# Performance work log

Measured on AMD Instinct MI355X. Metric: run time of the kernel, lower is better.

## Reference

```python
import jax, jax.numpy as jnp
import numpy as np

G = 8          # num_groups
GIN = 2048 // G   # group_in_features
GOUT = 2048 // G  # group_out_features


def setup_inputs() -> dict:
    key = jax.random.key(0)
    kx, kw, kb = jax.random.split(key, 3)
    x = jax.random.normal(kx, (8192, 2048), dtype=jnp.float32)
    # per-group linear params, torch nn.Linear default init scale ~ U(-1/sqrt(fan_in), ...)
    bound = 1.0 / np.sqrt(GIN)
    W = jax.random.uniform(kw, (G, GIN, GOUT), minval=-bound, maxval=bound, dtype=jnp.float32)
    b = jax.random.uniform(kb, (G, GOUT), minval=-bound, maxval=bound, dtype=jnp.float32)
    # rational activation coeffs, init p=[1,0,0,0], q=[1,0,0] per group
    p = jnp.tile(jnp.array([1.0, 0.0, 0.0, 0.0], dtype=jnp.float32), (G, 1))
    q = jnp.tile(jnp.array([1.0, 0.0, 0.0], dtype=jnp.float32), (G, 1))
    return {"x": x, "W": W, "b": b, "p": p, "q": q}


def _rational(y, p, q):
    # y: [N, G, GOUT]; p: [G, 4]; q: [G, 3] -> broadcast over N and GOUT
    p = p[None, :, :, None]  # [1,G,4,1]
    q = q[None, :, :, None]  # [1,G,3,1]
    y2 = y * y
    y3 = y2 * y
    num = p[:, :, 0] + p[:, :, 1] * y + p[:, :, 2] * y2 + p[:, :, 3] * y3
    den = 1.0 + jnp.abs(q[:, :, 0] * y + q[:, :, 1] * y2 + q[:, :, 2] * y3)
    return num / den


def reference(x, W, b, p, q):
    N = x.shape[0]
    xg = x.reshape(N, G, GIN)                       # chunk along last dim
    y = jnp.einsum('ngi,gio->ngo', xg, W) + b[None]  # grouped GEMM, [N,G,GOUT]
    out = _rational(y, p, q)
    return out.reshape(N, G * GOUT)                 # cat along last dim
```

## Files before the change

kernel.cpp:

```cpp
#include <hip/hip_runtime.h>
#include <hip/hip_bf16.h>

#define G_ 8
#define GIN_ 256
#define GOUT_ 256
#define NROWS_ 8192
#define LDX_ 2048

typedef __attribute__((ext_vector_type(4))) float f32x4;
typedef __attribute__((ext_vector_type(8))) short bf16x8;

__global__ __launch_bounds__(256) void wprep_kernel(const float* __restrict__ W,
                                                    __hip_bfloat16* __restrict__ Wt) {
    __shared__ float tile[64][65];
    const int bid = blockIdx.x;
    const int g  = bid >> 4;
    const int kt = (bid >> 2) & 3;
    const int ct = bid & 3;
    const float* Wg = W + g * (GIN_ * GOUT_);
    __hip_bfloat16* Wo = Wt + (size_t)g * (GIN_ * GOUT_);
    const int lane_o = threadIdx.x & 63;
    const int sub    = threadIdx.x >> 6;
#pragma unroll
    for (int r = 0; r < 16; ++r) {
        int i = r * 4 + sub;
        tile[i][lane_o] = Wg[(kt * 64 + i) * GOUT_ + ct * 64 + lane_o];
    }
    __syncthreads();
    const int col = threadIdx.x & 63;
    const int kgb = threadIdx.x >> 6;
#pragma unroll
    for (int h = 0; h < 2; ++h) {
        const int kg    = kgb + h * 4;
        const int kglob = kt * 64 + kg * 8;
        const int c     = kglob >> 5;
        const int quad  = (kglob >> 3) & 3;
        const int colg  = ct * 64 + col;
        const int cb    = colg >> 4;
        const int c16   = colg & 15;
        union { __hip_bfloat16 hh[8]; bf16x8 v; } cv;
#pragma unroll
        for (int j = 0; j < 8; ++j)
            cv.hh[j] = __float2bfloat16(tile[kg * 8 + j][col]);
        *(bf16x8*)(Wo + (size_t)(c * 16 + cb) * 512 + c16 * 32 + quad * 8) = cv.v;
    }
}

__device__ __forceinline__ bf16x8 cvt8(const f32x4 a, const f32x4 b) {
    union { __hip_bfloat16 h[8]; bf16x8 v; } u;
    u.h[0] = __float2bfloat16(a.x); u.h[1] = __float2bfloat16(a.y);
    u.h[2] = __float2bfloat16(a.z); u.h[3] = __float2bfloat16(a.w);
    u.h[4] = __float2bfloat16(b.x); u.h[5] = __float2bfloat16(b.y);
    u.h[6] = __float2bfloat16(b.z); u.h[7] = __float2bfloat16(b.w);
    return u.v;
}

__global__ __launch_bounds__(512, 8) void gkan_kernel(const float* __restrict__ x,
                                                      const __hip_bfloat16* __restrict__ Wt,
                                                      const float* __restrict__ bias,
                                                      const float* __restrict__ pc,
                                                      const float* __restrict__ qc,
                                                      float* __restrict__ out) {
    __shared__ __align__(16) float As[32 * 256];

    const int bid  = blockIdx.x;
    const int g    = bid & 7;
    const int row0 = (bid >> 3) * 32;

    const int t    = threadIdx.x;
    const int wave = t >> 6;
    const int lane = t & 63;
    const int lm   = lane & 15;
    const int q    = lane >> 4;

    {
        const float* xrow = x + (size_t)row0 * LDX_ + g * GIN_;
#pragma unroll
        for (int r = 0; r < 4; ++r) {
            const int row  = r * 8 + wave;
            const int gidx = lane ^ wave;
            const float* src = xrow + (size_t)row * LDX_ + gidx * 4;
            __builtin_amdgcn_global_load_lds(
                (const __attribute__((address_space(1))) void*)src,
                (__attribute__((address_space(3))) void*)((char*)As + r * 8192 + t * 16),
                16, 0, 0);
        }
    }

    asm volatile("s_waitcnt vmcnt(0) lgkmcnt(0)\n\ts_barrier" ::: "memory");

    f32x4 acc[2][2] = {};
    const __hip_bfloat16* bp = Wt + (size_t)g * (GIN_ * GOUT_)
                                  + (wave * 2) * 512 + lm * 32 + q * 8;
#pragma unroll 1
    for (int c = 0; c < 8; ++c) {
        const bf16x8 bf0 = *(const bf16x8*)(bp);
        const bf16x8 bf1 = *(const bf16x8*)(bp + 512);
        const int s0 = c * 8 + q * 2;
        bf16x8 af[2];
#pragma unroll
        for (int mt = 0; mt < 2; ++mt) {
            const int rr = mt * 16 + lm;
            const f32x4 lo = *(const f32x4*)(As + rr * 256 + ((s0 ^ (lm & 7)) * 4));
            const f32x4 hi = *(const f32x4*)(As + rr * 256 + (((s0 + 1) ^ (lm & 7)) * 4));
            af[mt] = cvt8(lo, hi);
        }
        acc[0][0] = __builtin_amdgcn_mfma_f32_16x16x32_bf16(bf0, af[0], acc[0][0], 0, 0, 0);
        acc[0][1] = __builtin_amdgcn_mfma_f32_16x16x32_bf16(bf1, af[0], acc[0][1], 0, 0, 0);
        acc[1][0] = __builtin_amdgcn_mfma_f32_16x16x32_bf16(bf0, af[1], acc[1][0], 0, 0, 0);
        acc[1][1] = __builtin_amdgcn_mfma_f32_16x16x32_bf16(bf1, af[1], acc[1][1], 0, 0, 0);
        bp += 16 * 512;
    }

    const float p0 = pc[g * 4 + 0], p1 = pc[g * 4 + 1];
    const float p2 = pc[g * 4 + 2], p3 = pc[g * 4 + 3];
    const float q0 = qc[g * 3 + 0], q1 = qc[g * 3 + 1], q2 = qc[g * 3 + 2];

#pragma unroll
    for (int mt = 0; mt < 2; ++mt) {
        const int row_o = row0 + mt * 16 + lm;
#pragma unroll
        for (int nt = 0; nt < 2; ++nt) {
            const int col0 = g * GOUT_ + wave * 32 + nt * 16 + q * 4;
            const f32x4 bb4 = *(const f32x4*)(bias + col0);
            f32x4 o;
#pragma unroll
            for (int r = 0; r < 4; ++r) {
                const float y   = acc[mt][nt][r] + bb4[r];
                const float num = p0 + y * (p1 + y * (p2 + y * p3));
                const float den = 1.0f + fabsf(y * (q0 + y * (q1 + y * q2)));
                o[r] = num * __builtin_amdgcn_rcpf(den);
            }
            *(f32x4*)(out + (size_t)row_o * LDX_ + col0) = o;
        }
    }
}

extern "C" void kernel_launch(void* const* d_in, const int* in_sizes, int n_in,
                              void* d_out, int out_size, void* d_ws, size_t ws_size,
                              hipStream_t stream) {
    const float* x = (const float*)d_in[0];
    const float* W = (const float*)d_in[1];
    const float* b = (const float*)d_in[2];
    const float* p = (const float*)d_in[3];
    const float* q = (const float*)d_in[4];
    float* out = (float*)d_out;

    __hip_bfloat16* Wt = (__hip_bfloat16*)d_ws;

    wprep_kernel<<<128, 256, 0, stream>>>(W, Wt);
    gkan_kernel<<<2048, 512, 0, stream>>>(x, Wt, b, p, q, out);
}
```

Measured before the change: 134.4 us.

## Split K into two halves and prefetch B fragments to overlap loads with MFMA

Hoists the bf16 weight-fragment loads ahead of the x tile copy into registers, and reorganises the global-to-LDS copy so each half of K lands in its own LDS region. Compute on the first half starts after a partial vmcnt wait while the second half is still in flight, and the second-half B fragments are loaded during the first half's MFMAs. The occupancy hint drops from 8 to 6 waves-per-EU to make room for the extra fragment registers. The cost is more register pressure, lower occupancy, and waitcnt counts that depend on the exact order of issued loads.

```diff
diff --git a/kernel.cpp b/kernel.cpp
--- a/kernel.cpp
+++ b/kernel.cpp
@@ -55,7 +55,7 @@
     return u.v;
 }
 
-__global__ __launch_bounds__(512, 8) void gkan_kernel(const float* __restrict__ x,
+__global__ __launch_bounds__(512, 6) void gkan_kernel(const float* __restrict__ x,
                                                       const __hip_bfloat16* __restrict__ Wt,
                                                       const float* __restrict__ bias,
                                                       const float* __restrict__ pc,
@@ -73,43 +73,80 @@
     const int lm   = lane & 15;
     const int q    = lane >> 4;
 
+    const __hip_bfloat16* bp = Wt + (size_t)g * (GIN_ * GOUT_)
+                                  + (wave * 2) * 512 + lm * 32 + q * 8;
+    bf16x8 B0[4], B1[4];
+#pragma unroll
+    for (int c = 0; c < 4; ++c) {
+        B0[c] = *(const bf16x8*)(bp + (size_t)c * (16 * 512));
+        B1[c] = *(const bf16x8*)(bp + (size_t)c * (16 * 512) + 512);
+    }
+
     {
         const float* xrow = x + (size_t)row0 * LDX_ + g * GIN_;
+        const int rw  = t >> 5;
+        const int g8  = t & 7;
+        const int ghi = t & 24;
 #pragma unroll
-        for (int r = 0; r < 4; ++r) {
-            const int row  = r * 8 + wave;
-            const int gidx = lane ^ wave;
-            const float* src = xrow + (size_t)row * LDX_ + gidx * 4;
-            __builtin_amdgcn_global_load_lds(
-                (const __attribute__((address_space(1))) void*)src,
-                (__attribute__((address_space(3))) void*)((char*)As + r * 8192 + t * 16),
-                16, 0, 0);
-        }
+        for (int h = 0; h < 2; ++h)
+#pragma unroll
+            for (int j = 0; j < 2; ++j) {
+                const int row  = j * 16 + rw;
+                const int gsrc = h * 32 + ghi + (g8 ^ (row & 7));
+                const float* src = xrow + (size_t)row * LDX_ + gsrc * 4;
+                __builtin_amdgcn_global_load_lds(
+                    (const __attribute__((address_space(1))) void*)src,
+                    (__attribute__((address_space(3))) void*)
+                        ((char*)As + h * 16384 + j * 8192 + t * 16),
+                    16, 0, 0);
+            }
     }
 
-    asm volatile("s_waitcnt vmcnt(0) lgkmcnt(0)\n\ts_barrier" ::: "memory");
+    asm volatile("s_waitcnt vmcnt(2)\n\ts_barrier" ::: "memory");
 
     f32x4 acc[2][2] = {};
-    const __hip_bfloat16* bp = Wt + (size_t)g * (GIN_ * GOUT_)
-                                  + (wave * 2) * 512 + lm * 32 + q * 8;
-#pragma unroll 1
-    for (int c = 0; c < 8; ++c) {
-        const bf16x8 bf0 = *(const bf16x8*)(bp);
-        const bf16x8 bf1 = *(const bf16x8*)(bp + 512);
-        const int s0 = c * 8 + q * 2;
+#pragma unroll
+    for (int c = 0; c < 4; ++c) {
         bf16x8 af[2];
 #pragma unroll
         for (int mt = 0; mt < 2; ++mt) {
-            const int rr = mt * 16 + lm;
-            const f32x4 lo = *(const f32x4*)(As + rr * 256 + ((s0 ^ (lm & 7)) * 4));
-            const f32x4 hi = *(const f32x4*)(As + rr * 256 + (((s0 + 1) ^ (lm & 7)) * 4));
+            const int rr  = mt * 16 + lm;
+            const int gg0 = c * 8 + ((q * 2)     ^ (lm & 7));
+            const int gg1 = c * 8 + ((q * 2 + 1) ^ (lm & 7));
+            const f32x4 lo = *(const f32x4*)((const char*)As + rr * 512 + gg0 * 16);
+            const f32x4 hi = *(const f32x4*)((const char*)As + rr * 512 + gg1 * 16);
             af[mt] = cvt8(lo, hi);
         }
-        acc[0][0] = __builtin_amdgcn_mfma_f32_16x16x32_bf16(bf0, af[0], acc[0][0], 0, 0, 0);
-        acc[0][1] = __builtin_amdgcn_mfma_f32_16x16x32_bf16(bf1, af[0], acc[0][1], 0, 0, 0);
-        acc[1][0] = __builtin_amdgcn_mfma_f32_16x16x32_bf16(bf0, af[1], acc[1][0], 0, 0, 0);
-        acc[1][1] = __builtin_amdgcn_mfma_f32_16x16x32_bf16(bf1, af[1], acc[1][1], 0, 0, 0);
-        bp += 16 * 512;
+        acc[0][0] = __builtin_amdgcn_mfma_f32_16x16x32_bf16(B0[c], af[0], acc[0][0], 0, 0, 0);
+        acc[0][1] = __builtin_amdgcn_mfma_f32_16x16x32_bf16(B1[c], af[0], acc[0][1], 0, 0, 0);
+        acc[1][0] = __builtin_amdgcn_mfma_f32_16x16x32_bf16(B0[c], af[1], acc[1][0], 0, 0, 0);
+        acc[1][1] = __builtin_amdgcn_mfma_f32_16x16x32_bf16(B1[c], af[1], acc[1][1], 0, 0, 0);
+    }
+
+#pragma unroll
+    for (int c = 0; c < 4; ++c) {
+        B0[c] = *(const bf16x8*)(bp + (size_t)(c + 4) * (16 * 512));
+        B1[c] = *(const bf16x8*)(bp + (size_t)(c + 4) * (16 * 512) + 512);
+    }
+
+    asm volatile("s_waitcnt vmcnt(8)\n\ts_barrier" ::: "memory");
+
+#pragma unroll
+    for (int c = 0; c < 4; ++c) {
+        bf16x8 af[2];
+#pragma unroll
+        for (int mt = 0; mt < 2; ++mt) {
+            const int rr  = mt * 16 + lm;
+            const int gg0 = c * 8 + ((q * 2)     ^ (lm & 7));
+            const int gg1 = c * 8 + ((q * 2 + 1) ^ (lm & 7));
+            const f32x4 lo = *(const f32x4*)((const char*)As + 16384 + rr * 512 + gg0 * 16);
+            const f32x4 hi = *(const f32x4*)((const char*)As + 16384 + rr * 512 + gg1 * 16);
+            af[mt] = cvt8(lo, hi);
+        }
+        acc[0][0] = __builtin_amdgcn_mfma_f32_16x16x32_bf16(B0[c], af[0], acc[0][0], 0, 0, 0);
+        acc[0][1] = __builtin_amdgcn_mfma_f32_16x16x32_bf16(B1[c], af[0], acc[0][1], 0, 0, 0);
+        acc[1][0] = __builtin_amdgcn_mfma_f32_16x16x32_bf16(B0[c], af[1], acc[1][0], 0, 0, 0);
+        acc[1][1] = __builtin_amdgcn_mfma_f32_16x16x32_bf16(B1[c], af[1], acc[1][1], 0, 0, 0);
     }
 
     const float p0 = pc[g * 4 + 0], p1 = pc[g * 4 + 1];
```

Measured after the change: 134.1 us. No clear change (-0.2%).

## Restructure GEMM so each block covers all groups for 16 full rows

Applied to the files above, without the earlier changes.

Each block now loads 16 full rows of x (all 8 groups) through registers, converts them to bf16 once, and stores them to a swizzled LDS tile. Each wave then handles one group and computes all 256 output columns in two passes of 8 MFMA accumulators. Before, x was kept as fp32 in LDS and converted on every read. The grid shrinks from 2048 to 512 blocks and the occupancy hint drops, so there is less latency hiding and more register pressure. It also drops the async global-to-LDS load path and reads far more W per wave from global or L2.

```diff
diff --git a/kernel.cpp b/kernel.cpp
--- a/kernel.cpp
+++ b/kernel.cpp
@@ -9,6 +9,10 @@
 
 typedef __attribute__((ext_vector_type(4))) float f32x4;
 typedef __attribute__((ext_vector_type(8))) short bf16x8;
+
+__device__ __forceinline__ void lds_barrier() {
+    asm volatile("s_waitcnt lgkmcnt(0)\n\ts_barrier" ::: "memory");
+}
 
 __global__ __launch_bounds__(256) void wprep_kernel(const float* __restrict__ W,
                                                     __hip_bfloat16* __restrict__ Wt) {
@@ -46,92 +50,84 @@
     }
 }
 
-__device__ __forceinline__ bf16x8 cvt8(const f32x4 a, const f32x4 b) {
-    union { __hip_bfloat16 h[8]; bf16x8 v; } u;
-    u.h[0] = __float2bfloat16(a.x); u.h[1] = __float2bfloat16(a.y);
-    u.h[2] = __float2bfloat16(a.z); u.h[3] = __float2bfloat16(a.w);
-    u.h[4] = __float2bfloat16(b.x); u.h[5] = __float2bfloat16(b.y);
-    u.h[6] = __float2bfloat16(b.z); u.h[7] = __float2bfloat16(b.w);
-    return u.v;
-}
-
-__global__ __launch_bounds__(512, 8) void gkan_kernel(const float* __restrict__ x,
+__global__ __launch_bounds__(512, 4) void gkan_kernel(const float* __restrict__ x,
                                                       const __hip_bfloat16* __restrict__ Wt,
                                                       const float* __restrict__ bias,
                                                       const float* __restrict__ pc,
                                                       const float* __restrict__ qc,
                                                       float* __restrict__ out) {
-    __shared__ __align__(16) float As[32 * 256];
+    __shared__ __align__(16) __hip_bfloat16 As[16 * 2048];
 
     const int bid  = blockIdx.x;
-    const int g    = bid & 7;
-    const int row0 = (bid >> 3) * 32;
+    const int row0 = bid * 16;
 
     const int t    = threadIdx.x;
-    const int wave = t >> 6;
+    const int w    = t >> 6;
     const int lane = t & 63;
     const int lm   = lane & 15;
     const int q    = lane >> 4;
 
     {
-        const float* xrow = x + (size_t)row0 * LDX_ + g * GIN_;
+        const float* xb = x + (size_t)row0 * LDX_ + t * 4;
+        f32x4 v[16];
 #pragma unroll
-        for (int r = 0; r < 4; ++r) {
-            const int row  = r * 8 + wave;
-            const int gidx = lane ^ wave;
-            const float* src = xrow + (size_t)row * LDX_ + gidx * 4;
-            __builtin_amdgcn_global_load_lds(
-                (const __attribute__((address_space(1))) void*)src,
-                (__attribute__((address_space(3))) void*)((char*)As + r * 8192 + t * 16),
-                16, 0, 0);
+        for (int r = 0; r < 16; ++r)
+            v[r] = *(const f32x4*)(xb + (size_t)r * LDX_);
+
+        const int gk   = t >> 1;
+        const int half = t & 1;
+#pragma unroll
+        for (int i = 0; i < 16; ++i) {
+            const int r = i ^ (gk & 7);
+            union { __hip_bfloat16 h[4]; uint2 u2; } cv;
+            cv.h[0] = __float2bfloat16(v[r].x);
+            cv.h[1] = __float2bfloat16(v[r].y);
+            cv.h[2] = __float2bfloat16(v[r].z);
+            cv.h[3] = __float2bfloat16(v[r].w);
+            const int phys = (gk & ~7) | ((gk & 7) ^ (r & 7));
+            *(uint2*)((char*)As + r * 4096 + phys * 16 + half * 8) = cv.u2;
         }
     }
+    lds_barrier();
 
-    asm volatile("s_waitcnt vmcnt(0) lgkmcnt(0)\n\ts_barrier" ::: "memory");
+    const float p0 = pc[w * 4 + 0], p1 = pc[w * 4 + 1];
+    const float p2 = pc[w * 4 + 2], p3 = pc[w * 4 + 3];
+    const float q0 = qc[w * 3 + 0], q1 = qc[w * 3 + 1], q2 = qc[w * 3 + 2];
 
-    f32x4 acc[2][2] = {};
-    const __hip_bfloat16* bp = Wt + (size_t)g * (GIN_ * GOUT_)
-                                  + (wave * 2) * 512 + lm * 32 + q * 8;
+    const char* ab = (const char*)As + lm * 4096 + w * 512;
+
 #pragma unroll 1
-    for (int c = 0; c < 8; ++c) {
-        const bf16x8 bf0 = *(const bf16x8*)(bp);
-        const bf16x8 bf1 = *(const bf16x8*)(bp + 512);
-        const int s0 = c * 8 + q * 2;
-        bf16x8 af[2];
+    for (int p = 0; p < 2; ++p) {
+        f32x4 acc[8] = {};
+        const __hip_bfloat16* bp = Wt + (size_t)w * (GIN_ * GOUT_)
+                                      + (size_t)(p * 8) * 512 + lm * 32 + q * 8;
+#pragma unroll 1
+        for (int c = 0; c < 8; ++c) {
+            const int gg   = c * 4 + q;
+            const int phys = (gg & 24) | ((gg & 7) ^ (lm & 7));
+            const bf16x8 af = *(const bf16x8*)(ab + phys * 16);
+            const __hip_bfloat16* bc = bp + (size_t)c * (16 * 512);
 #pragma unroll
-        for (int mt = 0; mt < 2; ++mt) {
-            const int rr = mt * 16 + lm;
-            const f32x4 lo = *(const f32x4*)(As + rr * 256 + ((s0 ^ (lm & 7)) * 4));
-            const f32x4 hi = *(const f32x4*)(As + rr * 256 + (((s0 + 1) ^ (lm & 7)) * 4));
-            af[mt] = cvt8(lo, hi);
+            for (int nt = 0; nt < 8; ++nt) {
+                const bf16x8 bf = *(const bf16x8*)(bc + nt * 512);
+                acc[nt] = __builtin_amdgcn_mfma_f32_16x16x32_bf16(bf, af, acc[nt], 0, 0, 0);
+            }
         }
-        acc[0][0] = __builtin_amdgcn_mfma_f32_16x16x32_bf16(bf0, af[0], acc[0][0], 0, 0, 0);
-        acc[0][1] = __builtin_amdgcn_mfma_f32_16x16x32_bf16(bf1, af[0], acc[0][1], 0, 0, 0);
-        acc[1][0] = __builtin_amdgcn_mfma_f32_16x16x32_bf16(bf0, af[1], acc[1][0], 0, 0, 0);
-        acc[1][1] = __builtin_amdgcn_mfma_f32_16x16x32_bf16(bf1, af[1], acc[1][1], 0, 0, 0);
-        bp += 16 * 512;
-    }
 
-    const float p0 = pc[g * 4 + 0], p1 = pc[g * 4 + 1];
-    const float p2 = pc[g * 4 + 2], p3 = pc[g * 4 + 3];
-    const float q0 = qc[g * 3 + 0], q1 = qc[g * 3 + 1], q2 = qc[g * 3 + 2];
-
+        const int colb = w * GOUT_ + p * 128;
 #pragma unroll
-    for (int mt = 0; mt < 2; ++mt) {
-        const int row_o = row0 + mt * 16 + lm;
-#pragma unroll
-        for (int nt = 0; nt < 2; ++nt) {
-            const int col0 = g * GOUT_ + wave * 32 + nt * 16 + q * 4;
+        for (int nt = 0; nt < 8; ++nt) {
+            const int col0 = colb + nt * 16 + q * 4;
             const f32x4 bb4 = *(const f32x4*)(bias + col0);
             f32x4 o;
 #pragma unroll
             for (int r = 0; r < 4; ++r) {
-                const float y   = acc[mt][nt][r] + bb4[r];
+                const float y   = acc[nt][r] + bb4[r];
                 const float num = p0 + y * (p1 + y * (p2 + y * p3));
                 const float den = 1.0f + fabsf(y * (q0 + y * (q1 + y * q2)));
                 o[r] = num * __builtin_amdgcn_rcpf(den);
             }
-            *(f32x4*)(out + (size_t)row_o * LDX_ + col0) = o;
+            *(f32x4*)(out + (size_t)(row0 + lm) * LDX_ + col0) = o;
         }
     }
 }
@@ -149,5 +145,5 @@
     __hip_bfloat16* Wt = (__hip_bfloat16*)d_ws;
 
     wprep_kernel<<<128, 256, 0, stream>>>(W, Wt);
-    gkan_kernel<<<2048, 512, 0, stream>>>(x, Wt, b, p, q, out);
+    gkan_kernel<<<512, 512, 0, stream>>>(x, Wt, b, p, q, out);
 }
```

Result: slower. 187.9 us (+39.8%).

## Double-buffer x slabs per block and keep W fragments in registers

Applied to the files above, without the earlier changes.

Each block now handles 128 rows as four 32-row slabs instead of a single slab. The next slab is prefetched into a second LDS buffer with global_load_lds while the current one is computed and its epilogue stored. The block's W fragments, bias and rational coefficients are loaded into registers once and reused across all four slabs, which cuts redundant weight loads. In exchange the grid shrinks to a quarter, so there are fewer blocks per CU and less latency hiding from occupancy, and register and LDS use per block rise.

```diff
diff --git a/kernel.cpp b/kernel.cpp
--- a/kernel.cpp
+++ b/kernel.cpp
@@ -55,17 +55,17 @@
     return u.v;
 }
 
-__global__ __launch_bounds__(512, 8) void gkan_kernel(const float* __restrict__ x,
+__global__ __launch_bounds__(512, 4) void gkan_kernel(const float* __restrict__ x,
                                                       const __hip_bfloat16* __restrict__ Wt,
                                                       const float* __restrict__ bias,
                                                       const float* __restrict__ pc,
                                                       const float* __restrict__ qc,
                                                       float* __restrict__ out) {
-    __shared__ __align__(16) float As[32 * 256];
+    __shared__ __align__(16) float As[2][32 * 256];
 
     const int bid  = blockIdx.x;
     const int g    = bid & 7;
-    const int row0 = (bid >> 3) * 32;
+    const int row0 = (bid >> 3) * 128;
 
     const int t    = threadIdx.x;
     const int wave = t >> 6;
@@ -73,67 +73,94 @@
     const int lm   = lane & 15;
     const int q    = lane >> 4;
 
-    {
-        const float* xrow = x + (size_t)row0 * LDX_ + g * GIN_;
-#pragma unroll
-        for (int r = 0; r < 4; ++r) {
-            const int row  = r * 8 + wave;
-            const int gidx = lane ^ wave;
-            const float* src = xrow + (size_t)row * LDX_ + gidx * 4;
-            __builtin_amdgcn_global_load_lds(
-                (const __attribute__((address_space(1))) void*)src,
-                (__attribute__((address_space(3))) void*)((char*)As + r * 8192 + t * 16),
-                16, 0, 0);
-        }
+    const float* xbase = x + (size_t)row0 * LDX_ + g * GIN_;
+    const int gsrc = (lane & ~7) | ((lane & 7) ^ wave);
+
+#define DMA_SLAB(s, buf)                                                      \
+    {                                                                         \
+        const float* xs_ = xbase + (size_t)(s) * 32 * LDX_;                   \
+        _Pragma("unroll")                                                     \
+        for (int r_ = 0; r_ < 4; ++r_) {                                      \
+            const float* src_ = xs_ + (size_t)(r_ * 8 + wave) * LDX_ + gsrc * 4; \
+            __builtin_amdgcn_global_load_lds(                                 \
+                (const __attribute__((address_space(1))) void*)src_,          \
+                (__attribute__((address_space(3))) void*)                     \
+                    ((char*)As + (buf) * 32768 + r_ * 8192 + t * 16),         \
+                16, 0, 0);                                                    \
+        }                                                                     \
     }
 
-    asm volatile("s_waitcnt vmcnt(0) lgkmcnt(0)\n\ts_barrier" ::: "memory");
+    DMA_SLAB(0, 0);
 
-    f32x4 acc[2][2] = {};
     const __hip_bfloat16* bp = Wt + (size_t)g * (GIN_ * GOUT_)
                                   + (wave * 2) * 512 + lm * 32 + q * 8;
-#pragma unroll 1
+    bf16x8 B0[8], B1[8];
+#pragma unroll
     for (int c = 0; c < 8; ++c) {
-        const bf16x8 bf0 = *(const bf16x8*)(bp);
-        const bf16x8 bf1 = *(const bf16x8*)(bp + 512);
-        const int s0 = c * 8 + q * 2;
-        bf16x8 af[2];
-#pragma unroll
-        for (int mt = 0; mt < 2; ++mt) {
-            const int rr = mt * 16 + lm;
-            const f32x4 lo = *(const f32x4*)(As + rr * 256 + ((s0 ^ (lm & 7)) * 4));
-            const f32x4 hi = *(const f32x4*)(As + rr * 256 + (((s0 + 1) ^ (lm & 7)) * 4));
-            af[mt] = cvt8(lo, hi);
-        }
-        acc[0][0] = __builtin_amdgcn_mfma_f32_16x16x32_bf16(bf0, af[0], acc[0][0], 0, 0, 0);
-        acc[0][1] = __builtin_amdgcn_mfma_f32_16x16x32_bf16(bf1, af[0], acc[0][1], 0, 0, 0);
-        acc[1][0] = __builtin_amdgcn_mfma_f32_16x16x32_bf16(bf0, af[1], acc[1][0], 0, 0, 0);
-        acc[1][1] = __builtin_amdgcn_mfma_f32_16x16x32_bf16(bf1, af[1], acc[1][1], 0, 0, 0);
-        bp += 16 * 512;
+        B0[c] = *(const bf16x8*)(bp + (size_t)c * (16 * 512));
+        B1[c] = *(const bf16x8*)(bp + (size_t)c * (16 * 512) + 512);
     }
 
+    f32x4 bb4[2];
+    int col0[2];
+#pragma unroll
+    for (int nt = 0; nt < 2; ++nt) {
+        col0[nt] = g * GOUT_ + wave * 32 + nt * 16 + q * 4;
+        bb4[nt]  = *(const f32x4*)(bias + col0[nt]);
+    }
     const float p0 = pc[g * 4 + 0], p1 = pc[g * 4 + 1];
     const float p2 = pc[g * 4 + 2], p3 = pc[g * 4 + 3];
     const float q0 = qc[g * 3 + 0], q1 = qc[g * 3 + 1], q2 = qc[g * 3 + 2];
 
+    asm volatile("s_waitcnt vmcnt(0)\n\ts_barrier" ::: "memory");
+
+#pragma unroll 1
+    for (int s = 0; s < 4; ++s) {
+        const int buf = s & 1;
+
+        if (s < 3) DMA_SLAB(s + 1, buf ^ 1);
+
+        f32x4 acc[2][2] = {};
+        const char* ab = (const char*)As + buf * 32768;
 #pragma unroll
-    for (int mt = 0; mt < 2; ++mt) {
-        const int row_o = row0 + mt * 16 + lm;
+        for (int c = 0; c < 8; ++c) {
+            bf16x8 af[2];
 #pragma unroll
-        for (int nt = 0; nt < 2; ++nt) {
-            const int col0 = g * GOUT_ + wave * 32 + nt * 16 + q * 4;
-            const f32x4 bb4 = *(const f32x4*)(bias + col0);
-            f32x4 o;
+            for (int mt = 0; mt < 2; ++mt) {
+                const int rr  = mt * 16 + lm;
+                const int gg0 = c * 8 + ((q * 2)     ^ (lm & 7));
+                const int gg1 = c * 8 + ((q * 2 + 1) ^ (lm & 7));
+                const f32x4 lo = *(const f32x4*)(ab + rr * 1024 + gg0 * 16);
+                const f32x4 hi = *(const f32x4*)(ab + rr * 1024 + gg1 * 16);
+                af[mt] = cvt8(lo, hi);
+            }
+            acc[0][0] = __builtin_amdgcn_mfma_f32_16x16x32_bf16(B0[c], af[0], acc[0][0], 0, 0, 0);
+            acc[0][1] = __builtin_amdgcn_mfma_f32_16x16x32_bf16(B1[c], af[0], acc[0][1], 0, 0, 0);
+            acc[1][0] = __builtin_amdgcn_mfma_f32_16x16x32_bf16(B0[c], af[1], acc[1][0], 0, 0, 0);
+            acc[1][1] = __builtin_amdgcn_mfma_f32_16x16x32_bf16(B1[c], af[1], acc[1][1], 0, 0, 0);
+        }
+
 #pragma unroll
-            for (int r = 0; r < 4; ++r) {
-                const float y   = acc[mt][nt][r] + bb4[r];
-                const float num = p0 + y * (p1 + y * (p2 + y * p3));
-                const float den = 1.0f + fabsf(y * (q0 + y * (q1 + y * q2)));
-                o[r] = num * __builtin_amdgcn_rcpf(den);
+        for (int mt = 0; mt < 2; ++mt) {
+            const int row_o = row0 + s * 32 + mt * 16 + lm;
+#pragma unroll
+            for (int nt = 0; nt < 2; ++nt) {
+                f32x4 o;
+#pragma unroll
+                for (int r = 0; r < 4; ++r) {
+                    const float y   = acc[mt][nt][r] + bb4[nt][r];
+                    const float num = p0 + y * (p1 + y * (p2 + y * p3));
+                    const float den = 1.0f + fabsf(y * (q0 + y * (q1 + y * q2)));
+                    o[r] = num * __builtin_amdgcn_rcpf(den);
+                }
+                *(f32x4*)(out + (size_t)row_o * LDX_ + col0[nt]) = o;
             }
-            *(f32x4*)(out + (size_t)row_o * LDX_ + col0) = o;
         }
+
+        if (s < 3)
+            asm volatile("s_waitcnt vmcnt(4)\n\ts_barrier" ::: "memory");
     }
+#undef DMA_SLAB
 }
 
 extern "C" void kernel_launch(void* const* d_in, const int* in_sizes, int n_in,
@@ -149,5 +176,5 @@
     __hip_bfloat16* Wt = (__hip_bfloat16*)d_ws;
 
     wprep_kernel<<<128, 256, 0, stream>>>(W, Wt);
-    gkan_kernel<<<2048, 512, 0, stream>>>(x, Wt, b, p, q, out);
+    gkan_kernel<<<512, 512, 0, stream>>>(x, Wt, b, p, q, out);
 }
```

Result: faster. 127.3 us (-5.3%).
